# Performance work log

Measured on AMD Instinct MI355X. Metric: run time of the kernel, lower is better.

The kernel has to match this reference:

```python
import jax, jax.numpy as jnp
import numpy as np

NUM_CLUSTERS = 64  # label vocabulary size (labels in [0, NUM_CLUSTERS))


def setup_inputs() -> dict:
    key = jax.random.key(0)
    kf, kl = jax.random.split(key)
    features = jax.random.normal(kf, (8192, 128), dtype=jnp.float32)
    labels = jax.random.randint(kl, (8192,), 0, NUM_CLUSTERS, dtype=jnp.int64)
    return {"features": features, "labels": labels}


def _pairwise_dist(x):
    # Euclidean cdist with a grad-safe sqrt (zero entries -> zero, no NaN grads).
    sq = jnp.sum(x * x, axis=-1)                      # [N]
    d2 = sq[:, None] + sq[None, :] - 2.0 * (x @ x.T)  # [N, N]
    d2 = jnp.maximum(d2, 0.0)
    pos = d2 > 0
    return jnp.sqrt(jnp.where(pos, d2, 1.0)) * pos.astype(x.dtype)


def reference(features, labels):
    N = features.shape[0]
    C = NUM_CLUSTERS
    dtype = features.dtype

    onehot = jax.nn.one_hot(labels, C, dtype=dtype)   # [N, C]
    counts = jnp.sum(onehot, axis=0)                  # [C]

    dists = _pairwise_dist(features)                  # [N, N]
    # Per-sample sum of distances to each cluster: segment-sum over columns.
    S = dists @ onehot                                # [N, C]

    own_count = counts[labels]                        # [N]
    idx = jnp.arange(N)
    # mean intra-cluster distance a_i (exclude self: divide by n-1)
    a = S[idx, labels] / jnp.maximum(own_count - 1.0, 1.0)

    # mean distance to every other cluster; mask own cluster and empty clusters
    mean_inter = S / jnp.maximum(counts, 1.0)[None, :]          # [N, C]
    invalid = (onehot > 0) | (counts[None, :] == 0)
    big = jnp.asarray(jnp.finfo(dtype).max, dtype)
    b = jnp.min(jnp.where(invalid, big, mean_inter), axis=1)    # [N]

    score = (b - a) / jnp.maximum(b, a)
    # singleton clusters get score 0 (matches torch branch num_elements <= 1)
    score = jnp.where(own_count > 1, score, jnp.zeros((), dtype))
    return jnp.mean(score)
```

## Files before the change

kernel.cpp:

```cpp
#include <hip/hip_runtime.h>
#include <hip/hip_fp16.h>
#include <float.h>

#define NC 64
#define FD 128
#define LSTR 136

typedef _Float16 f16x8 __attribute__((ext_vector_type(8)));
typedef float f32x4 __attribute__((ext_vector_type(4)));

__global__ void prep_kernel(const float* __restrict__ feat,
                            const int* __restrict__ labels,
                            float* __restrict__ sq,
                            unsigned short* __restrict__ Xh,
                            unsigned short* __restrict__ Mt,
                            float* __restrict__ S,
                            float* __restrict__ out, int out_size,
                            int* __restrict__ counts, int N) {
  __shared__ int hist[NC];
  int t = threadIdx.x;
  if (t < NC) hist[t] = 0;
  __syncthreads();
  int row = blockIdx.x * 32 + (t >> 3);
  int o = t & 7;
  if (row < N) {
    const float* rp = feat + (size_t)row * FD;
    float s = 0.f;
#pragma unroll
    for (int j = 0; j < 4; ++j) {
      int c4 = o + 8 * j;
      float4 v = *(const float4*)(rp + c4 * 4);
      ushort4 h;
      h.x = __half_as_ushort(__float2half(v.x));
      h.y = __half_as_ushort(__float2half(v.y));
      h.z = __half_as_ushort(__float2half(v.z));
      h.w = __half_as_ushort(__float2half(v.w));
      *(ushort4*)&Xh[(size_t)row * FD + c4 * 4] = h;
      s = fmaf(v.x, v.x, s); s = fmaf(v.y, v.y, s);
      s = fmaf(v.z, v.z, s); s = fmaf(v.w, v.w, s);
    }
    s += __shfl_xor(s, 1); s += __shfl_xor(s, 2); s += __shfl_xor(s, 4);
    if (o == 0) { sq[row] = s; atomicAdd(&hist[labels[row]], 1); }
  }
  if ((blockIdx.x + 1) * 32 <= N) {
    float4 z = {0.f, 0.f, 0.f, 0.f};
    size_t base = (size_t)blockIdx.x * 32 * NC + t * 8;
    *(float4*)&S[base] = z;
    *(float4*)&S[base + 4] = z;
  }
  if (blockIdx.x == 0 && t < out_size) out[t] = 0.f;
  {
    int chunksPerN = N >> 3;
    int total = NC * chunksPerN;
    for (int id = blockIdx.x * 256 + t; id < total; id += gridDim.x * 256) {
      int n = id / chunksPerN;
      int c0 = (id - n * chunksPerN) * 8;
      ushort4 lo, hi;
      lo.x = (labels[c0 + 0] == n) ? 0x3C00 : 0;
      lo.y = (labels[c0 + 1] == n) ? 0x3C00 : 0;
      lo.z = (labels[c0 + 2] == n) ? 0x3C00 : 0;
      lo.w = (labels[c0 + 3] == n) ? 0x3C00 : 0;
      hi.x = (labels[c0 + 4] == n) ? 0x3C00 : 0;
      hi.y = (labels[c0 + 5] == n) ? 0x3C00 : 0;
      hi.z = (labels[c0 + 6] == n) ? 0x3C00 : 0;
      hi.w = (labels[c0 + 7] == n) ? 0x3C00 : 0;
      *(ushort4*)&Mt[(size_t)n * N + c0] = lo;
      *(ushort4*)&Mt[(size_t)n * N + c0 + 4] = hi;
    }
  }
  __syncthreads();
  if (t < NC) atomicAdd(&counts[t], hist[t]);
}

__global__ __launch_bounds__(256, 2)
void mfma_tile_kernel(const unsigned short* __restrict__ Xh,
                      const float* __restrict__ sq,
                      const unsigned short* __restrict__ Mt,
                      float* __restrict__ S,
                      int N, int colsPerSplit) {
  __shared__ __align__(16) unsigned short Ah[128 * LSTR];
  __shared__ __align__(16) unsigned short Bh[128 * LSTR];

  const int t = threadIdx.x;
  const int R = blockIdx.x * 128;
  const int cBeg = blockIdx.y * colsPerSplit;
  const int wave = t >> 6, lane = t & 63;
  const int mm = lane & 15, quad = lane >> 4;
  const int wr = wave >> 1, wc = wave & 1;

#pragma unroll
  for (int it = 0; it < 8; ++it) {
    int c = t + it * 256;
    int r = c >> 4, k0 = (c & 15) * 8;
    *(uint4*)&Ah[r * LSTR + k0] = *(const uint4*)&Xh[(size_t)(R + r) * FD + k0];
  }
  float sqi_r[4];
#pragma unroll
  for (int ib = 0; ib < 4; ++ib)
    sqi_r[ib] = sq[R + wr * 64 + ib * 16 + mm];

  f32x4 sacc[2][4];
#pragma unroll
  for (int rt = 0; rt < 2; ++rt)
#pragma unroll
    for (int lt = 0; lt < 4; ++lt) sacc[rt][lt] = (f32x4)0.f;

  const int numTiles = colsPerSplit / 128;
  for (int ct = 0; ct < numTiles; ++ct) {
    const int C0 = cBeg + ct * 128;
    __syncthreads();
#pragma unroll
    for (int it = 0; it < 8; ++it) {
      int c = t + it * 256;
      int r = c >> 4, k0 = (c & 15) * 8;
      *(uint4*)&Bh[r * LSTR + k0] = *(const uint4*)&Xh[(size_t)(C0 + r) * FD + k0];
    }
    float sjr[4][4];
#pragma unroll
    for (int jb = 0; jb < 4; ++jb)
#pragma unroll
      for (int r = 0; r < 4; ++r)
        sjr[jb][r] = sq[C0 + wc * 64 + jb * 16 + quad * 4 + r];
    __syncthreads();

    f32x4 dacc[4][4];
#pragma unroll
    for (int ib = 0; ib < 4; ++ib)
#pragma unroll
      for (int jb = 0; jb < 4; ++jb) dacc[ib][jb] = (f32x4)0.f;

#pragma unroll
    for (int ks = 0; ks < 4; ++ks) {
      const int ko = ks * 32 + quad * 8;
      f16x8 af[4], bf[4];
#pragma unroll
      for (int ib = 0; ib < 4; ++ib)
        af[ib] = *(const f16x8*)&Ah[(wr * 64 + ib * 16 + mm) * LSTR + ko];
#pragma unroll
      for (int jb = 0; jb < 4; ++jb)
        bf[jb] = *(const f16x8*)&Bh[(wc * 64 + jb * 16 + mm) * LSTR + ko];
#pragma unroll
      for (int ib = 0; ib < 4; ++ib)
#pragma unroll
        for (int jb = 0; jb < 4; ++jb)
          dacc[ib][jb] = __builtin_amdgcn_mfma_f32_16x16x32_f16(bf[jb], af[ib], dacc[ib][jb], 0, 0, 0);
    }
    __syncthreads();

    const bool hasDiag = (R == C0);
#pragma unroll
    for (int ib = 0; ib < 4; ++ib) {
      const int rowLocal = wr * 64 + ib * 16 + mm;
      const float si = sqi_r[ib];
#pragma unroll
      for (int jb = 0; jb < 4; ++jb) {
        const int colBase = wc * 64 + jb * 16 + quad * 4;
        float d[4];
#pragma unroll
        for (int r = 0; r < 4; ++r) {
          float d2 = fmaf(-2.f, dacc[ib][jb][r], si + sjr[jb][r]);
          d[r] = __builtin_amdgcn_sqrtf(fmaxf(d2, 0.f));
        }
        if (hasDiag) {
#pragma unroll
          for (int r = 0; r < 4; ++r)
            if (rowLocal == colBase + r) d[r] = 0.f;
        }
        uint2 pk;
        pk.x = __builtin_bit_cast(unsigned, __builtin_amdgcn_cvt_pkrtz(d[0], d[1]));
        pk.y = __builtin_bit_cast(unsigned, __builtin_amdgcn_cvt_pkrtz(d[2], d[3]));
        *(uint2*)&Bh[rowLocal * LSTR + colBase] = pk;
      }
    }
    __syncthreads();

#pragma unroll
    for (int ks = 0; ks < 4; ++ks) {
      const int ko = ks * 32 + quad * 8;
      f16x8 da0 = *(const f16x8*)&Bh[(wave * 32 + mm) * LSTR + ko];
      f16x8 da1 = *(const f16x8*)&Bh[(wave * 32 + 16 + mm) * LSTR + ko];
#pragma unroll
      for (int lt = 0; lt < 4; ++lt) {
        f16x8 mb = *(const f16x8*)&Mt[(size_t)(lt * 16 + mm) * N + C0 + ks * 32 + quad * 8];
        sacc[0][lt] = __builtin_amdgcn_mfma_f32_16x16x32_f16(da0, mb, sacc[0][lt], 0, 0, 0);
        sacc[1][lt] = __builtin_amdgcn_mfma_f32_16x16x32_f16(da1, mb, sacc[1][lt], 0, 0, 0);
      }
    }
  }

#pragma unroll
  for (int rt = 0; rt < 2; ++rt)
#pragma unroll
    for (int lt = 0; lt < 4; ++lt)
#pragma unroll
      for (int r = 0; r < 4; ++r) {
        int row = wave * 32 + rt * 16 + quad * 4 + r;
        atomicAdd(&S[(size_t)(R + row) * NC + lt * 16 + mm], sacc[rt][lt][r]);
      }
}

__global__ void score_kernel(const float* __restrict__ S,
                             const int* __restrict__ labels,
                             const int* __restrict__ counts,
                             float* __restrict__ out, int N) {
  __shared__ float cnt_s[NC];
  __shared__ float inv_s[NC];
  __shared__ float red[128];
  int t = threadIdx.x;
  if (t < NC) {
    float c = (float)counts[t];
    cnt_s[t] = c;
    inv_s[t] = 1.f / fmaxf(c, 1.f);
  }
  __syncthreads();
  int i = blockIdx.x * 128 + t;
  float score = 0.f;
  if (i < N) {
    int li = labels[i];
    float own = cnt_s[li];
    const float4* Sv = (const float4*)(S + (size_t)i * NC);
    float a = S[(size_t)i * NC + li] / fmaxf(own - 1.f, 1.f);
    float b = FLT_MAX;
#pragma unroll
    for (int c4 = 0; c4 < NC / 4; ++c4) {
      float4 v = Sv[c4];
      int c = c4 * 4;
      float m0 = v.x * inv_s[c + 0];
      float m1 = v.y * inv_s[c + 1];
      float m2 = v.z * inv_s[c + 2];
      float m3 = v.w * inv_s[c + 3];
      b = fminf(b, (c + 0 == li || cnt_s[c + 0] == 0.f) ? FLT_MAX : m0);
      b = fminf(b, (c + 1 == li || cnt_s[c + 1] == 0.f) ? FLT_MAX : m1);
      b = fminf(b, (c + 2 == li || cnt_s[c + 2] == 0.f) ? FLT_MAX : m2);
      b = fminf(b, (c + 3 == li || cnt_s[c + 3] == 0.f) ? FLT_MAX : m3);
    }
    float mx = fmaxf(a, b);
    score = (own > 1.f) ? (b - a) / mx : 0.f;
  }
  red[t] = score;
  __syncthreads();
  for (int sft = 64; sft > 0; sft >>= 1) {
    if (t < sft) red[t] += red[t + sft];
    __syncthreads();
  }
  if (t == 0) atomicAdd(out, red[0] / (float)N);
}

extern "C" void kernel_launch(void* const* d_in, const int* in_sizes, int n_in,
                              void* d_out, int out_size, void* d_ws, size_t ws_size,
                              hipStream_t stream) {
  const float* feat = (const float*)d_in[0];
  const int* labels = (const int*)d_in[1];
  const int N = in_sizes[1];
  float* out = (float*)d_out;
  char* ws = (char*)d_ws;

  int*   counts = (int*)ws;
  float* sq     = (float*)(ws + 256);
  size_t o = 256 + (size_t)N * 4;
  o = (o + 255) & ~(size_t)255;
  unsigned short* Xh = (unsigned short*)(ws + o);
  unsigned short* Mt = (unsigned short*)(ws + o + (size_t)N * FD * 2);
  float* S = (float*)(ws + o + (size_t)N * FD * 2 + (size_t)NC * N * 2);

  (void)hipMemsetAsync(counts, 0, 256, stream);

  prep_kernel<<<(N + 31) / 32, 256, 0, stream>>>(feat, labels, sq, Xh, Mt, S,
                                                 out, out_size, counts, N);

  const int colSplit = 8;
  dim3 grid(N / 128, colSplit);
  mfma_tile_kernel<<<grid, 256, 0, stream>>>(Xh, sq, Mt, S, N, N / colSplit);

  score_kernel<<<(N + 127) / 128, 128, 0, stream>>>(S, labels, counts, out, N);
}
```

Before: 125.3 us.

## Fuse score pass into tile kernel via last-block election and prefetch B tiles

The separate score kernel and the counts memset are removed. The last column-split block of each row group, found with a done-counter atomic, rebuilds the label histogram in shared memory and computes and reduces the silhouette scores itself. The B-tile global loads are also staged through registers one tile ahead, so they overlap with the MFMA work of the current tile. This saves a kernel launch and a memset but adds threadfences, atomic loads and a redundant histogram pass over all labels in each finishing block, plus extra register pressure from the prefetch buffer.

```diff
diff --git a/kernel.cpp b/kernel.cpp
--- a/kernel.cpp
+++ b/kernel.cpp
@@ -15,12 +15,9 @@
                             unsigned short* __restrict__ Xh,
                             unsigned short* __restrict__ Mt,
                             float* __restrict__ S,
-                            float* __restrict__ out, int out_size,
-                            int* __restrict__ counts, int N) {
-  __shared__ int hist[NC];
+                            int* __restrict__ done,
+                            float* __restrict__ out, int out_size, int N) {
   int t = threadIdx.x;
-  if (t < NC) hist[t] = 0;
-  __syncthreads();
   int row = blockIdx.x * 32 + (t >> 3);
   int o = t & 7;
   if (row < N) {
@@ -40,7 +37,7 @@
       s = fmaf(v.z, v.z, s); s = fmaf(v.w, v.w, s);
     }
     s += __shfl_xor(s, 1); s += __shfl_xor(s, 2); s += __shfl_xor(s, 4);
-    if (o == 0) { sq[row] = s; atomicAdd(&hist[labels[row]], 1); }
+    if (o == 0) sq[row] = s;
   }
   if ((blockIdx.x + 1) * 32 <= N) {
     float4 z = {0.f, 0.f, 0.f, 0.f};
@@ -48,7 +45,10 @@
     *(float4*)&S[base] = z;
     *(float4*)&S[base + 4] = z;
   }
-  if (blockIdx.x == 0 && t < out_size) out[t] = 0.f;
+  if (blockIdx.x == 0) {
+    if (t < N / 128) done[t] = 0;
+    if (t < out_size) out[t] = 0.f;
+  }
   {
     int chunksPerN = N >> 3;
     int total = NC * chunksPerN;
@@ -68,18 +68,20 @@
       *(ushort4*)&Mt[(size_t)n * N + c0 + 4] = hi;
     }
   }
-  __syncthreads();
-  if (t < NC) atomicAdd(&counts[t], hist[t]);
 }
 
 __global__ __launch_bounds__(256, 2)
 void mfma_tile_kernel(const unsigned short* __restrict__ Xh,
                       const float* __restrict__ sq,
                       const unsigned short* __restrict__ Mt,
+                      const int* __restrict__ labels,
                       float* __restrict__ S,
+                      int* __restrict__ done,
+                      float* __restrict__ out,
                       int N, int colsPerSplit) {
   __shared__ __align__(16) unsigned short Ah[128 * LSTR];
   __shared__ __align__(16) unsigned short Bh[128 * LSTR];
+  __shared__ int lastFlag;
 
   const int t = threadIdx.x;
   const int R = blockIdx.x * 128;
@@ -88,12 +90,17 @@
   const int mm = lane & 15, quad = lane >> 4;
   const int wr = wave >> 1, wc = wave & 1;
 
-#pragma unroll
-  for (int it = 0; it < 8; ++it) {
-    int c = t + it * 256;
-    int r = c >> 4, k0 = (c & 15) * 8;
-    *(uint4*)&Ah[r * LSTR + k0] = *(const uint4*)&Xh[(size_t)(R + r) * FD + k0];
-  }
+  const int sr = t >> 4, sk0 = (t & 15) * 8;
+#pragma unroll
+  for (int it = 0; it < 8; ++it)
+    *(uint4*)&Ah[(sr + it * 16) * LSTR + sk0] =
+        *(const uint4*)&Xh[(size_t)(R + sr + it * 16) * FD + sk0];
+
+  uint4 bpref[8];
+#pragma unroll
+  for (int it = 0; it < 8; ++it)
+    bpref[it] = *(const uint4*)&Xh[(size_t)(cBeg + sr + it * 16) * FD + sk0];
+
   float sqi_r[4];
 #pragma unroll
   for (int ib = 0; ib < 4; ++ib)
@@ -110,11 +117,12 @@
     const int C0 = cBeg + ct * 128;
     __syncthreads();
 #pragma unroll
-    for (int it = 0; it < 8; ++it) {
-      int c = t + it * 256;
-      int r = c >> 4, k0 = (c & 15) * 8;
-      *(uint4*)&Bh[r * LSTR + k0] = *(const uint4*)&Xh[(size_t)(C0 + r) * FD + k0];
-    }
+    for (int it = 0; it < 8; ++it)
+      *(uint4*)&Bh[(sr + it * 16) * LSTR + sk0] = bpref[it];
+    const int nC0 = (ct + 1 < numTiles) ? C0 + 128 : cBeg;
+#pragma unroll
+    for (int it = 0; it < 8; ++it)
+      bpref[it] = *(const uint4*)&Xh[(size_t)(nC0 + sr + it * 16) * FD + sk0];
     float sjr[4][4];
 #pragma unroll
     for (int jb = 0; jb < 4; ++jb)
@@ -197,49 +205,49 @@
         int row = wave * 32 + rt * 16 + quad * 4 + r;
         atomicAdd(&S[(size_t)(R + row) * NC + lt * 16 + mm], sacc[rt][lt][r]);
       }
-}
-
-__global__ void score_kernel(const float* __restrict__ S,
-                             const int* __restrict__ labels,
-                             const int* __restrict__ counts,
-                             float* __restrict__ out, int N) {
-  __shared__ float cnt_s[NC];
-  __shared__ float inv_s[NC];
-  __shared__ float red[128];
-  int t = threadIdx.x;
-  if (t < NC) {
-    float c = (float)counts[t];
-    cnt_s[t] = c;
-    inv_s[t] = 1.f / fmaxf(c, 1.f);
-  }
-  __syncthreads();
-  int i = blockIdx.x * 128 + t;
+
+  __threadfence();
+  __syncthreads();
+  if (t == 0) {
+    int old = atomicAdd(&done[blockIdx.x], 1);
+    lastFlag = (old == (int)gridDim.y - 1) ? 1 : 0;
+  }
+  __syncthreads();
+  if (!lastFlag) return;
+  __threadfence();
+
+  int* hist = (int*)Ah;
+  float* red = (float*)Bh;
+  if (t < NC) hist[t] = 0;
+  __syncthreads();
+  const int4* lab4 = (const int4*)labels;
+  for (int i = t; i < N / 4; i += 256) {
+    int4 v = lab4[i];
+    atomicAdd(&hist[v.x], 1); atomicAdd(&hist[v.y], 1);
+    atomicAdd(&hist[v.z], 1); atomicAdd(&hist[v.w], 1);
+  }
+  __syncthreads();
+
   float score = 0.f;
-  if (i < N) {
+  if (t < 128) {
+    int i = R + t;
     int li = labels[i];
-    float own = cnt_s[li];
-    const float4* Sv = (const float4*)(S + (size_t)i * NC);
-    float a = S[(size_t)i * NC + li] / fmaxf(own - 1.f, 1.f);
-    float b = FLT_MAX;
-#pragma unroll
-    for (int c4 = 0; c4 < NC / 4; ++c4) {
-      float4 v = Sv[c4];
-      int c = c4 * 4;
-      float m0 = v.x * inv_s[c + 0];
-      float m1 = v.y * inv_s[c + 1];
-      float m2 = v.z * inv_s[c + 2];
-      float m3 = v.w * inv_s[c + 3];
-      b = fminf(b, (c + 0 == li || cnt_s[c + 0] == 0.f) ? FLT_MAX : m0);
-      b = fminf(b, (c + 1 == li || cnt_s[c + 1] == 0.f) ? FLT_MAX : m1);
-      b = fminf(b, (c + 2 == li || cnt_s[c + 2] == 0.f) ? FLT_MAX : m2);
-      b = fminf(b, (c + 3 == li || cnt_s[c + 3] == 0.f) ? FLT_MAX : m3);
+    float own = (float)hist[li];
+    float a = 0.f, b = FLT_MAX;
+    const float* Si = S + (size_t)i * NC;
+#pragma unroll
+    for (int c = 0; c < NC; ++c) {
+      float s = __hip_atomic_load(&Si[c], __ATOMIC_RELAXED, __HIP_MEMORY_SCOPE_AGENT);
+      float cf = (float)hist[c];
+      if (c == li) a = s / fmaxf(own - 1.f, 1.f);
+      else if (cf != 0.f) b = fminf(b, s / cf);
     }
     float mx = fmaxf(a, b);
     score = (own > 1.f) ? (b - a) / mx : 0.f;
   }
   red[t] = score;
   __syncthreads();
-  for (int sft = 64; sft > 0; sft >>= 1) {
+  for (int sft = 128; sft > 0; sft >>= 1) {
     if (t < sft) red[t] += red[t + sft];
     __syncthreads();
   }
@@ -255,22 +263,19 @@
   float* out = (float*)d_out;
   char* ws = (char*)d_ws;
 
-  int*   counts = (int*)ws;
-  float* sq     = (float*)(ws + 256);
+  int*   done = (int*)ws;
+  float* sq   = (float*)(ws + 256);
   size_t o = 256 + (size_t)N * 4;
   o = (o + 255) & ~(size_t)255;
   unsigned short* Xh = (unsigned short*)(ws + o);
   unsigned short* Mt = (unsigned short*)(ws + o + (size_t)N * FD * 2);
   float* S = (float*)(ws + o + (size_t)N * FD * 2 + (size_t)NC * N * 2);
 
-  (void)hipMemsetAsync(counts, 0, 256, stream);
-
   prep_kernel<<<(N + 31) / 32, 256, 0, stream>>>(feat, labels, sq, Xh, Mt, S,
-                                                 out, out_size, counts, N);
+                                                 done, out, out_size, N);
 
   const int colSplit = 8;
   dim3 grid(N / 128, colSplit);
-  mfma_tile_kernel<<<grid, 256, 0, stream>>>(Xh, sq, Mt, S, N, N / colSplit);
-
-  score_kernel<<<(N + 127) / 128, 128, 0, stream>>>(S, labels, counts, out, N);
+  mfma_tile_kernel<<<grid, 256, 0, stream>>>(Xh, sq, Mt, labels, S, done, out,
+                                             N, N / colSplit);
 }
```

Result: slower. 186.2 us (+48.6%).
